# Kernel tuning notes

Measured on AMD Instinct MI355X. Metric: run time of the kernel, lower is better.

Reference implementation:

```python
import jax, jax.numpy as jnp
import numpy as np

EMBED_DIM = 1024
NUM_HEADS = 16
HEAD_DIM = 64
B, S = 4, 2048


def setup_inputs() -> dict:
    key = jax.random.key(0)
    ks = jax.random.split(key, 5)
    std = 0.02
    x = jax.random.normal(ks[0], (B, S, EMBED_DIM), dtype=jnp.float32)
    Wq = std * jax.random.normal(ks[1], (NUM_HEADS, EMBED_DIM, HEAD_DIM), dtype=jnp.float32)
    Wk = std * jax.random.normal(ks[2], (NUM_HEADS, EMBED_DIM, HEAD_DIM), dtype=jnp.float32)
    Wv = std * jax.random.normal(ks[3], (NUM_HEADS, EMBED_DIM, HEAD_DIM), dtype=jnp.float32)
    Wo = std * jax.random.normal(ks[4], (NUM_HEADS, HEAD_DIM, EMBED_DIM), dtype=jnp.float32)
    bq = jnp.zeros((NUM_HEADS, HEAD_DIM), dtype=jnp.float32)
    bk = jnp.zeros((NUM_HEADS, HEAD_DIM), dtype=jnp.float32)
    bv = jnp.zeros((NUM_HEADS, HEAD_DIM), dtype=jnp.float32)
    bo = jnp.zeros((EMBED_DIM,), dtype=jnp.float32)
    return {"x": x, "Wq": Wq, "bq": bq, "Wk": Wk, "bk": bk,
            "Wv": Wv, "bv": bv, "Wo": Wo, "bo": bo}


def reference(x, Wq, bq, Wk, bk, Wv, bv, Wo, bo):
    # q,k,v: [b, s, n, h]
    q = jnp.einsum('bsd,ndh->bsnh', x, Wq) + bq
    k = jnp.einsum('bsd,ndh->bsnh', x, Wk) + bk
    v = jnp.einsum('bsd,ndh->bsnh', x, Wv) + bv
    scale = 1.0 / (HEAD_DIM ** 0.5)
    # non-causal full attention matrix [b, n, s, t]
    attn = jnp.einsum('bsnh,btnh->bnst', q, k) * scale
    attn = jax.nn.softmax(attn, axis=-1)
    after = jnp.einsum('bnst,btnh->bsnh', attn, v)
    out = jnp.einsum('bsnh,nhd->bsd', after, Wo) + bo
    return out
```

## Files before the change

### kernel.cpp

```cpp
#include <hip/hip_runtime.h>

typedef __bf16 bf16;
typedef bf16 bf16x8 __attribute__((ext_vector_type(8)));
typedef bf16 bf16x4 __attribute__((ext_vector_type(4)));
typedef bf16 bf16x2 __attribute__((ext_vector_type(2)));
typedef float f32x4 __attribute__((ext_vector_type(4)));
typedef float f32x16 __attribute__((ext_vector_type(16)));
typedef unsigned int u32;
typedef u32 u32x4 __attribute__((ext_vector_type(4)));
typedef int i32x2 __attribute__((ext_vector_type(2)));

constexpr int Bb = 4, Ss = 2048, Dd = 1024, NH = 16, HD = 64;
constexpr int BS = Bb * Ss;
constexpr float CSC = 0.18033688011112042f;

__device__ __forceinline__ int sw(int row, int col) {
  return (row << 6) + (col ^ ((row & 7) << 3));
}
__device__ __forceinline__ int sw128(int row, int col) {
  return (row << 7) + (col ^ ((row & 7) << 3));
}

__device__ __forceinline__ void g2l16(const bf16* g, bf16* l) {
  __builtin_amdgcn_global_load_lds(
      (const __attribute__((address_space(1))) void*)g,
      (__attribute__((address_space(3))) void*)l, 16, 0, 0);
}

__device__ __forceinline__ u32 pkbf(float a, float b) {
  bf16x2 v = {(bf16)a, (bf16)b};
  return __builtin_bit_cast(u32, v);
}

__global__ void prep(const float* __restrict__ x, bf16* __restrict__ xb,
                     const float* __restrict__ Wq, const float* __restrict__ Wk,
                     const float* __restrict__ Wv, const float* __restrict__ Wo,
                     const float* __restrict__ bq, const float* __restrict__ bk,
                     const float* __restrict__ bv,
                     bf16* __restrict__ WT_all, bf16* __restrict__ WoT,
                     float* __restrict__ bias_all) {
  __shared__ bf16 Ts[64 * 72];
  const int t = threadIdx.x;
  if (blockIdx.y == 0) {
    int o = (blockIdx.x * 256 + t) * 4;
    f32x4 v = *(const f32x4*)&x[o];
    bf16x4 r = {(bf16)v[0], (bf16)v[1], (bf16)v[2], (bf16)v[3]};
    *(bf16x4*)&xb[o] = r;
    return;
  }
  if (blockIdx.x > 1024) return;
  if (blockIdx.x == 1024) {
    for (int j = t; j < 3072; j += 256) {
      int s2 = j >> 10;
      const float* bb = (s2 == 0) ? bq : (s2 == 1) ? bk : bv;
      bias_all[j] = bb[j & 1023] * (s2 == 0 ? CSC : 1.0f);
    }
    return;
  }
  const int sel = blockIdx.x >> 8, bx = blockIdx.x & 255;
  if (sel < 3) {
    const float* W = (sel == 0) ? Wq : (sel == 1) ? Wk : Wv;
    float scale = (sel == 0) ? CSC : 1.0f;
    int head = bx >> 4, dt = bx & 15;
    const float* src = W + head * 65536 + dt * 64 * 64;
#pragma unroll
    for (int i = 0; i < 4; ++i) {
      int idx = i * 256 + t;
      int dr = idx >> 4, hc = (idx & 15) * 4;
      f32x4 v = *(const f32x4*)&src[dr * 64 + hc];
#pragma unroll
      for (int k = 0; k < 4; ++k) Ts[(hc + k) * 72 + dr] = (bf16)(v[k] * scale);
    }
    __syncthreads();
    bf16* dst = WT_all + (size_t)sel * 1048576 + (size_t)(head * 64) * 1024 + dt * 64;
#pragma unroll
    for (int i = 0; i < 2; ++i) {
      int idx = i * 256 + t;
      int hr = idx >> 3, ch = (idx & 7) * 8;
      *(bf16x8*)&dst[(size_t)hr * 1024 + ch] = *(const bf16x8*)&Ts[hr * 72 + ch];
    }
  } else {
    int ct = bx >> 4, dt = bx & 15;
    const float* src = Wo + (size_t)(ct * 64) * 1024 + dt * 64;
#pragma unroll
    for (int i = 0; i < 4; ++i) {
      int idx = i * 256 + t;
      int cr = idx >> 4, dc = (idx & 15) * 4;
      f32x4 v = *(const f32x4*)&src[(size_t)cr * 1024 + dc];
#pragma unroll
      for (int k = 0; k < 4; ++k) Ts[(dc + k) * 72 + cr] = (bf16)v[k];
    }
    __syncthreads();
    bf16* dst = WoT + (size_t)(dt * 64) * 1024 + ct * 64;
#pragma unroll
    for (int i = 0; i < 2; ++i) {
      int idx = i * 256 + t;
      int dr = idx >> 3, ch = (idx & 7) * 8;
      *(bf16x8*)&dst[(size_t)dr * 1024 + ch] = *(const bf16x8*)&Ts[dr * 72 + ch];
    }
  }
}

__device__ __forceinline__ void gemm_core(const bf16* __restrict__ A,
                                          const bf16* __restrict__ BT,
                                          int m0, int n0, bf16* As, bf16* Bs,
                                          f32x4 (&acc)[4][4]) {
  const int t = threadIdx.x;
  const int l = t & 63, q = l >> 4, lm = l & 15;
  const int w = t >> 6, wm = w & 1, wn = w >> 1;
  int ro[4], co[4];
#pragma unroll
  for (int i = 0; i < 4; ++i) {
    int o = i * 256 + t;
    ro[i] = o >> 3;
    co[i] = ((o & 7) ^ ((o >> 3) & 7)) << 3;
  }
  const int lbase = (t & 192) * 8;
  for (int k0 = 0; k0 < 1024; k0 += 64) {
    __syncthreads();
#pragma unroll
    for (int i = 0; i < 4; ++i)
      g2l16(&A[(size_t)(m0 + ro[i]) * 1024 + k0 + co[i]], &As[i * 2048 + lbase]);
#pragma unroll
    for (int i = 0; i < 4; ++i)
      g2l16(&BT[(size_t)(n0 + ro[i]) * 1024 + k0 + co[i]], &Bs[i * 2048 + lbase]);
    __syncthreads();
#pragma unroll
    for (int kh = 0; kh < 2; ++kh) {
      bf16x8 a[4], b[4];
#pragma unroll
      for (int i = 0; i < 4; ++i)
        a[i] = *(const bf16x8*)&As[sw(wm * 64 + i * 16 + lm, kh * 32 + q * 8)];
#pragma unroll
      for (int i = 0; i < 4; ++i)
        b[i] = *(const bf16x8*)&Bs[sw(wn * 64 + i * 16 + lm, kh * 32 + q * 8)];
#pragma unroll
      for (int mt = 0; mt < 4; ++mt)
#pragma unroll
        for (int nt = 0; nt < 4; ++nt)
          acc[mt][nt] = __builtin_amdgcn_mfma_f32_16x16x32_bf16(a[mt], b[nt], acc[mt][nt], 0, 0, 0);
    }
  }
}

__global__ __launch_bounds__(256) void gemm_qkv(const bf16* __restrict__ xb,
                                                const bf16* __restrict__ WT,
                                                const float* __restrict__ bias_all,
                                                bf16* __restrict__ QKb,
                                                bf16* __restrict__ VTb) {
  __shared__ __align__(16) bf16 SMEM[2 * 128 * 64];
  bf16* As = SMEM;
  bf16* Bs = SMEM + 128 * 64;
  const int bid = blockIdx.x;
  const int t = threadIdx.x;
  const int l = t & 63, q = l >> 4, lm = l & 15;
  const int w = t >> 6, wm = w & 1, wn = w >> 1;
  const bool vmode = bid >= 1024;
  int m0, n0;
  const bf16 *A, *BT;
  if (!vmode) {
    int xcd = bid & 7, idx = bid >> 3;
    m0 = (idx >> 1) * 128;
    n0 = (xcd * 2 + (idx & 1)) * 128;
    A = xb; BT = WT;
  } else {
    int b2 = bid - 1024;
    int xcd = b2 & 7, idx = b2 >> 3;
    m0 = (idx >> 3) * 128;
    n0 = (xcd * 8 + (idx & 7)) * 128;
    A = WT + (size_t)2048 * 1024; BT = xb;
  }
  f32x4 acc[4][4] = {};
  gemm_core(A, BT, m0, n0, As, Bs, acc);
  if (vmode) {
    __syncthreads();
#pragma unroll
    for (int nt = 0; nt < 4; ++nt) {
      int sl = wn * 64 + nt * 16 + lm;
#pragma unroll
      for (int mt = 0; mt < 4; ++mt) {
        int ml = wm * 64 + mt * 16 + q * 4;
#pragma unroll
        for (int r = 0; r < 4; ++r)
          SMEM[sw128(ml + r, sl)] = (bf16)(acc[mt][nt][r] + bias_all[2048 + m0 + ml + r]);
      }
    }
    __syncthreads();
    int hh = t >> 1, half = (t & 1) * 64;
    int m = m0 + hh;
    size_t gb = (size_t)((n0 >> 11) * 16 + (m >> 6)) * 131072 +
                (size_t)(m & 63) * 2048 + (n0 & 2047) + half;
#pragma unroll
    for (int k = 0; k < 8; ++k)
      *(bf16x8*)&VTb[gb + k * 8] = *(const bf16x8*)&SMEM[sw128(hh, half + k * 8)];
  } else {
#pragma unroll
    for (int nt = 0; nt < 4; ++nt) {
      int col = n0 + wn * 64 + nt * 16 + lm;
      float bb = bias_all[col];
#pragma unroll
      for (int mt = 0; mt < 4; ++mt) {
        int row = m0 + wm * 64 + mt * 16 + q * 4;
#pragma unroll
        for (int r = 0; r < 4; ++r)
          QKb[(size_t)(row + r) * 2048 + col] = (bf16)(acc[mt][nt][r] + bb);
      }
    }
  }
}

__global__ __launch_bounds__(256) void gemm_out(const bf16* __restrict__ after,
                                                const bf16* __restrict__ WoT,
                                                const float* __restrict__ bo,
                                                float* __restrict__ out) {
  __shared__ __align__(16) bf16 SMEM[2 * 128 * 64];
  const int bid = blockIdx.x;
  const int t = threadIdx.x;
  const int l = t & 63, q = l >> 4, lm = l & 15;
  const int w = t >> 6, wm = w & 1, wn = w >> 1;
  const int xcd = bid & 7, idx = bid >> 3;
  const int n0 = xcd * 128, m0 = idx * 128;
  f32x4 acc[4][4] = {};
  gemm_core(after, WoT, m0, n0, SMEM, SMEM + 128 * 64, acc);
#pragma unroll
  for (int nt = 0; nt < 4; ++nt) {
    int col = n0 + wn * 64 + nt * 16 + lm;
    float bb = bo[col];
#pragma unroll
    for (int mt = 0; mt < 4; ++mt) {
      int row = m0 + wm * 64 + mt * 16 + q * 4;
#pragma unroll
      for (int r = 0; r < 4; ++r)
        out[(size_t)(row + r) * 1024 + col] = acc[mt][nt][r] + bb;
    }
  }
}

__global__ __launch_bounds__(256, 2) void attn(const bf16* __restrict__ QK,
                                               const bf16* __restrict__ VT,
                                               bf16* __restrict__ after) {
  __shared__ __align__(16) bf16 SMEM[32768];
  const int t = threadIdx.x;
  const int l = t & 63, w = t >> 6;
  const int lh = l & 31, H = l >> 5;
  const int f = blockIdx.x;
  const int bn = (f & 7) | ((f >> 6) << 3);
  const int s0 = ((f >> 3) & 7) * 256;
  const int b = bn >> 4, n = bn & 15;
  const bf16* Qb = QK + (size_t)(b * 2048) * 2048 + n * 64;
  const bf16* Kb = Qb + 1024;
  const bf16* Vtb = VT + (size_t)bn * 131072;
  const int rr = t >> 3;
  const int co0 = ((t & 7) ^ (rr & 7)) << 3;
  const int lbase = (t & 192) * 8;
#pragma unroll
  for (int i = 0; i < 8; ++i)
    g2l16(&Qb[(size_t)(s0 + i * 32 + rr) * 2048 + co0], &SMEM[i * 2048 + lbase]);
  __syncthreads();
  bf16x8 qb[2][4];
#pragma unroll
  for (int qt = 0; qt < 2; ++qt)
#pragma unroll
    for (int ks = 0; ks < 4; ++ks)
      qb[qt][ks] = *(const bf16x8*)&SMEM[sw(w * 64 + qt * 32 + lh, ks * 16 + H * 8)];
  __syncthreads();
#pragma unroll
  for (int s = 0; s < 3; ++s)
#pragma unroll
    for (int i = 0; i < 2; ++i) {
      g2l16(&Kb[(size_t)(s * 64 + i * 32 + rr) * 2048 + co0],
            &SMEM[s * 4096 + i * 2048 + lbase]);
      g2l16(&Vtb[(size_t)(i * 32 + rr) * 2048 + s * 64 + co0],
            &SMEM[16384 + s * 4096 + i * 2048 + lbase]);
    }
  f32x16 o_acc[2][2] = {};
  float rsA[2] = {0.f, 0.f}, rsB[2] = {0.f, 0.f};
  for (int rd = 0; rd < 32; ++rd) {
    const int cur = rd & 3;
    const bf16* Ks = &SMEM[cur * 4096];
    const bf16* Vs = &SMEM[16384 + cur * 4096];
    if (rd < 30)       asm volatile("s_waitcnt vmcnt(8)" ::: "memory");
    else if (rd == 30) asm volatile("s_waitcnt vmcnt(4)" ::: "memory");
    else               asm volatile("s_waitcnt vmcnt(0)" ::: "memory");
    __builtin_amdgcn_s_barrier();
    __builtin_amdgcn_sched_barrier(0);
    if (rd <= 28) {
      int st = rd + 3, nb = st & 3, t0n = st * 64;
#pragma unroll
      for (int i = 0; i < 2; ++i) {
        g2l16(&Kb[(size_t)(t0n + i * 32 + rr) * 2048 + co0],
              &SMEM[nb * 4096 + i * 2048 + lbase]);
        g2l16(&Vtb[(size_t)(i * 32 + rr) * 2048 + t0n + co0],
              &SMEM[16384 + nb * 4096 + i * 2048 + lbase]);
      }
    }
#pragma unroll
    for (int tt = 0; tt < 2; ++tt) {
      bf16x8 kb[4];
#pragma unroll
      for (int ks = 0; ks < 4; ++ks)
        kb[ks] = *(const bf16x8*)&Ks[sw(tt * 32 + lh, ks * 16 + H * 8)];
      f32x16 sc[2] = {};
      __builtin_amdgcn_s_setprio(1);
#pragma unroll
      for (int ks = 0; ks < 4; ++ks)
#pragma unroll
        for (int qt = 0; qt < 2; ++qt)
          sc[qt] = __builtin_amdgcn_mfma_f32_32x32x16_bf16(kb[ks], qb[qt][ks], sc[qt], 0, 0, 0);
      __builtin_amdgcn_s_setprio(0);
      u32 pk[2][8];
#pragma unroll
      for (int qt = 0; qt < 2; ++qt)
#pragma unroll
        for (int i = 0; i < 8; ++i) {
          float p0 = __builtin_amdgcn_exp2f(sc[qt][2 * i]);
          float p1 = __builtin_amdgcn_exp2f(sc[qt][2 * i + 1]);
          rsA[qt] += p0;
          rsB[qt] += p1;
          pk[qt][i] = pkbf(p0, p1);
        }
#pragma unroll
      for (int ks2 = 0; ks2 < 2; ++ks2) {
        bf16x8 pa[2];
#pragma unroll
        for (int qt = 0; qt < 2; ++qt) {
          u32x4 av;
#if __has_builtin(__builtin_amdgcn_permlane32_swap)
          i32x2 sA = __builtin_amdgcn_permlane32_swap(
              (int)pk[qt][ks2 * 4 + 0], (int)pk[qt][ks2 * 4 + 2], false, false);
          i32x2 sB = __builtin_amdgcn_permlane32_swap(
              (int)pk[qt][ks2 * 4 + 1], (int)pk[qt][ks2 * 4 + 3], false, false);
          av[0] = (u32)sA[0]; av[1] = (u32)sB[0]; av[2] = (u32)sA[1]; av[3] = (u32)sB[1];
#else
          u32 xx[4];
          xx[0] = __shfl_xor((int)pk[qt][ks2 * 4 + 0], 32);
          xx[1] = __shfl_xor((int)pk[qt][ks2 * 4 + 1], 32);
          xx[2] = __shfl_xor((int)pk[qt][ks2 * 4 + 2], 32);
          xx[3] = __shfl_xor((int)pk[qt][ks2 * 4 + 3], 32);
          av[0] = H ? xx[2] : pk[qt][ks2 * 4 + 0];
          av[1] = H ? xx[3] : pk[qt][ks2 * 4 + 1];
          av[2] = H ? pk[qt][ks2 * 4 + 2] : xx[0];
          av[3] = H ? pk[qt][ks2 * 4 + 3] : xx[1];
#endif
          pa[qt] = __builtin_bit_cast(bf16x8, av);
        }
        __builtin_amdgcn_s_setprio(1);
#pragma unroll
        for (int ht = 0; ht < 2; ++ht) {
          bf16x8 vb = *(const bf16x8*)&Vs[sw(ht * 32 + lh, tt * 32 + ks2 * 16 + H * 8)];
#pragma unroll
          for (int qt = 0; qt < 2; ++qt)
            o_acc[qt][ht] = __builtin_amdgcn_mfma_f32_32x32x16_bf16(pa[qt], vb, o_acc[qt][ht], 0, 0, 0);
        }
        __builtin_amdgcn_s_setprio(0);
      }
    }
  }
#pragma unroll
  for (int qt = 0; qt < 2; ++qt) {
    float rs = rsA[qt] + rsB[qt];
    rs += __shfl_xor(rs, 32);
    float inv = 1.f / rs;
#pragma unroll
    for (int r = 0; r < 16; ++r) {
      int sl = (r & 3) + 8 * (r >> 2) + 4 * H;
      float invr = __shfl(inv, sl);
      size_t base = (size_t)(b * 2048 + s0 + w * 64 + qt * 32 + sl) * 1024 + n * 64;
#pragma unroll
      for (int ht = 0; ht < 2; ++ht)
        after[base + ht * 32 + lh] = (bf16)(o_acc[qt][ht][r] * invr);
    }
  }
}

extern "C" void kernel_launch(void* const* d_in, const int* in_sizes, int n_in,
                              void* d_out, int out_size, void* d_ws, size_t ws_size,
                              hipStream_t stream) {
  const float* x  = (const float*)d_in[0];
  const float* Wq = (const float*)d_in[1];
  const float* bq = (const float*)d_in[2];
  const float* Wk = (const float*)d_in[3];
  const float* bk = (const float*)d_in[4];
  const float* Wv = (const float*)d_in[5];
  const float* bv = (const float*)d_in[6];
  const float* Wo = (const float*)d_in[7];
  const float* bo = (const float*)d_in[8];
  float* out = (float*)d_out;

  bf16* WT_all    = (bf16*)d_ws;
  bf16* WoT       = WT_all + (size_t)3072 * 1024;
  float* bias_all = (float*)(WoT + (size_t)1024 * 1024);
  bf16* xb        = (bf16*)(bias_all + 4096);
  bf16* QKb       = xb + (size_t)BS * Dd;
  bf16* VTb       = QKb + (size_t)BS * 2048;
  bf16* after     = VTb + (size_t)Bb * NH * HD * Ss;

  prep<<<dim3(8192, 2), dim3(256), 0, stream>>>(x, xb, Wq, Wk, Wv, Wo, bq, bk, bv,
                                                WT_all, WoT, bias_all);
  gemm_qkv<<<dim3(1536), dim3(256), 0, stream>>>(xb, WT_all, bias_all, QKb, VTb);
  attn<<<dim3(512), dim3(256), 0, stream>>>(QKb, VTb, after);
  gemm_out<<<dim3(512), dim3(256), 0, stream>>>(after, WoT, bo, out);
}
```

Baseline: 278.5 us.

## Split QKV GEMM into 256x256-tile Q/K kernel with 8-wave pipelined schedule

Moves the Q/K projection into a new kernel that uses 256x256 output tiles, 512 threads, a 128KB double-buffered LDS layout, and staged loads interleaved with MFMA phases plus setprio hints. The V projection is split into its own launch. The larger tiles raise data reuse per loaded byte and the interleaved schedule is meant to hide global-load latency. The cost is an extra kernel launch, only 256 blocks for the Q/K grid, and heavy LDS use that limits occupancy.

New measurement: 264.9 us. 4.9% less time.

```diff
diff --git a/kernel.cpp b/kernel.cpp
--- a/kernel.cpp
+++ b/kernel.cpp
@@ -143,11 +143,161 @@
   }
 }
 
-__global__ __launch_bounds__(256) void gemm_qkv(const bf16* __restrict__ xb,
-                                                const bf16* __restrict__ WT,
-                                                const float* __restrict__ bias_all,
-                                                bf16* __restrict__ QKb,
-                                                bf16* __restrict__ VTb) {
+__global__ __launch_bounds__(512, 2) void gemm_qk8(const bf16* __restrict__ A,
+                                                   const bf16* __restrict__ BT,
+                                                   const float* __restrict__ bias_all,
+                                                   bf16* __restrict__ C) {
+  __shared__ __align__(16) bf16 SMEM[65536];
+  const int t = threadIdx.x;
+  const int l = t & 63, q = l >> 4, lm = l & 15;
+  const int w = t >> 6, wm = w & 1, wn = w >> 1;
+  const int bid = blockIdx.x;
+  const int xcd = bid & 7, cc = bid >> 3;
+  const int mt = xcd * 4 + (cc >> 3), nt = cc & 7;
+  const int m0 = mt * 256, n0 = nt * 256;
+  const bf16* Ag = A + (size_t)m0 * 1024;
+  const bf16* Bg = BT + (size_t)n0 * 1024;
+  const int sR = t >> 3;
+  const int sC = t & 7;
+  const int dstb = (t & 448) * 8;
+
+  auto stA = [&](int bufb, int h, int kt) {
+#pragma unroll
+    for (int i = 0; i < 2; ++i) {
+      int Lh = i * 64 + sR;
+      int gr = ((Lh >> 6) << 7) + h * 64 + (Lh & 63);
+      g2l16(&Ag[(size_t)gr * 1024 + kt * 64 + ((sC ^ (Lh & 7)) << 3)],
+            &SMEM[bufb * 32768 + h * 8192 + i * 4096 + dstb]);
+    }
+  };
+  auto stB = [&](int bufb, int h, int kt) {
+#pragma unroll
+    for (int i = 0; i < 2; ++i) {
+      int Lh = i * 64 + sR;
+      int gr = ((Lh >> 5) << 6) + h * 32 + (Lh & 31);
+      g2l16(&Bg[(size_t)gr * 1024 + kt * 64 + ((sC ^ (Lh & 7)) << 3)],
+            &SMEM[bufb * 32768 + 16384 + h * 8192 + i * 4096 + dstb]);
+    }
+  };
+  auto rdA = [&](int base, int mt16, int ks) {
+    int L = ((mt16 >> 2) << 7) + wm * 64 + ((mt16 & 3) << 4) + lm;
+    return *(const bf16x8*)&SMEM[base + sw(L, ks * 32 + q * 8)];
+  };
+  auto rdB = [&](int base, int nt16, int ks) {
+    int L = ((nt16 >> 1) << 7) + wn * 32 + ((nt16 & 1) << 4) + lm;
+    return *(const bf16x8*)&SMEM[base + 16384 + sw(L, ks * 32 + q * 8)];
+  };
+
+  stA(0, 0, 0); stA(0, 1, 0); stB(0, 0, 0); stB(0, 1, 0);
+  stA(1, 0, 1); stB(1, 0, 1);
+  asm volatile("s_waitcnt vmcnt(4)" ::: "memory");
+  __builtin_amdgcn_s_barrier();
+  __builtin_amdgcn_sched_barrier(0);
+
+  f32x4 acc[8][4] = {};
+  int cur = 0;
+  for (int kt = 0; kt < 16; ++kt, cur ^= 1) {
+    const int base = cur * 32768;
+    bf16x8 af[4][2], b0[2][2], b1[2][2];
+#pragma unroll
+    for (int mi = 0; mi < 4; ++mi)
+#pragma unroll
+      for (int ks = 0; ks < 2; ++ks) af[mi][ks] = rdA(base, mi, ks);
+#pragma unroll
+    for (int ni = 0; ni < 2; ++ni)
+#pragma unroll
+      for (int ks = 0; ks < 2; ++ks) b0[ni][ks] = rdB(base, ni, ks);
+    if (kt + 1 < 16) { stA(cur ^ 1, 1, kt + 1); stB(cur ^ 1, 1, kt + 1); }
+    __builtin_amdgcn_s_barrier();
+    __builtin_amdgcn_s_setprio(1);
+#pragma unroll
+    for (int mi = 0; mi < 4; ++mi)
+#pragma unroll
+      for (int ni = 0; ni < 2; ++ni)
+#pragma unroll
+        for (int ks = 0; ks < 2; ++ks)
+          acc[mi][ni] = __builtin_amdgcn_mfma_f32_16x16x32_bf16(af[mi][ks], b0[ni][ks], acc[mi][ni], 0, 0, 0);
+    __builtin_amdgcn_s_setprio(0);
+    __builtin_amdgcn_sched_barrier(0);
+    __builtin_amdgcn_s_barrier();
+    __builtin_amdgcn_sched_barrier(0);
+#pragma unroll
+    for (int ni = 0; ni < 2; ++ni)
+#pragma unroll
+      for (int ks = 0; ks < 2; ++ks) b1[ni][ks] = rdB(base, 2 + ni, ks);
+    __builtin_amdgcn_s_barrier();
+    __builtin_amdgcn_s_setprio(1);
+#pragma unroll
+    for (int mi = 0; mi < 4; ++mi)
+#pragma unroll
+      for (int ni = 0; ni < 2; ++ni)
+#pragma unroll
+        for (int ks = 0; ks < 2; ++ks)
+          acc[mi][2 + ni] = __builtin_amdgcn_mfma_f32_16x16x32_bf16(af[mi][ks], b1[ni][ks], acc[mi][2 + ni], 0, 0, 0);
+    __builtin_amdgcn_s_setprio(0);
+    __builtin_amdgcn_sched_barrier(0);
+    __builtin_amdgcn_s_barrier();
+    __builtin_amdgcn_sched_barrier(0);
+#pragma unroll
+    for (int mi = 0; mi < 4; ++mi)
+#pragma unroll
+      for (int ks = 0; ks < 2; ++ks) af[mi][ks] = rdA(base, 4 + mi, ks);
+#pragma unroll
+    for (int ni = 0; ni < 2; ++ni)
+#pragma unroll
+      for (int ks = 0; ks < 2; ++ks) b0[ni][ks] = rdB(base, ni, ks);
+    if (kt + 2 < 16) stA(cur, 0, kt + 2);
+    __builtin_amdgcn_s_barrier();
+    __builtin_amdgcn_s_setprio(1);
+#pragma unroll
+    for (int mi = 0; mi < 4; ++mi)
+#pragma unroll
+      for (int ni = 0; ni < 2; ++ni)
+#pragma unroll
+        for (int ks = 0; ks < 2; ++ks)
+          acc[4 + mi][ni] = __builtin_amdgcn_mfma_f32_16x16x32_bf16(af[mi][ks], b0[ni][ks], acc[4 + mi][ni], 0, 0, 0);
+    __builtin_amdgcn_s_setprio(0);
+    __builtin_amdgcn_sched_barrier(0);
+    __builtin_amdgcn_s_barrier();
+    __builtin_amdgcn_sched_barrier(0);
+#pragma unroll
+    for (int ni = 0; ni < 2; ++ni)
+#pragma unroll
+      for (int ks = 0; ks < 2; ++ks) b1[ni][ks] = rdB(base, 2 + ni, ks);
+    if (kt + 2 < 16) stB(cur, 0, kt + 2);
+    __builtin_amdgcn_s_barrier();
+    __builtin_amdgcn_s_setprio(1);
+#pragma unroll
+    for (int mi = 0; mi < 4; ++mi)
+#pragma unroll
+      for (int ni = 0; ni < 2; ++ni)
+#pragma unroll
+        for (int ks = 0; ks < 2; ++ks)
+          acc[4 + mi][2 + ni] = __builtin_amdgcn_mfma_f32_16x16x32_bf16(af[mi][ks], b1[ni][ks], acc[4 + mi][2 + ni], 0, 0, 0);
+    __builtin_amdgcn_s_setprio(0);
+    asm volatile("s_waitcnt vmcnt(4)" ::: "memory");
+    __builtin_amdgcn_sched_barrier(0);
+    __builtin_amdgcn_s_barrier();
+    __builtin_amdgcn_sched_barrier(0);
+  }
+#pragma unroll
+  for (int mi = 0; mi < 8; ++mi) {
+    int row = m0 + wm * 128 + mi * 16 + q * 4;
+#pragma unroll
+    for (int ni = 0; ni < 4; ++ni) {
+      int col = n0 + wn * 64 + ni * 16 + lm;
+      float bb = bias_all[col];
+#pragma unroll
+      for (int r = 0; r < 4; ++r)
+        C[(size_t)(row + r) * 2048 + col] = (bf16)(acc[mi][ni][r] + bb);
+    }
+  }
+}
+
+__global__ __launch_bounds__(256) void gemm_v(const bf16* __restrict__ xb,
+                                              const bf16* __restrict__ WT,
+                                              const float* __restrict__ bias_all,
+                                              bf16* __restrict__ VTb) {
   __shared__ __align__(16) bf16 SMEM[2 * 128 * 64];
   bf16* As = SMEM;
   bf16* Bs = SMEM + 128 * 64;
@@ -155,58 +305,33 @@
   const int t = threadIdx.x;
   const int l = t & 63, q = l >> 4, lm = l & 15;
   const int w = t >> 6, wm = w & 1, wn = w >> 1;
-  const bool vmode = bid >= 1024;
-  int m0, n0;
-  const bf16 *A, *BT;
-  if (!vmode) {
-    int xcd = bid & 7, idx = bid >> 3;
-    m0 = (idx >> 1) * 128;
-    n0 = (xcd * 2 + (idx & 1)) * 128;
-    A = xb; BT = WT;
-  } else {
-    int b2 = bid - 1024;
-    int xcd = b2 & 7, idx = b2 >> 3;
-    m0 = (idx >> 3) * 128;
-    n0 = (xcd * 8 + (idx & 7)) * 128;
-    A = WT + (size_t)2048 * 1024; BT = xb;
-  }
+  const int xcd = bid & 7, idx = bid >> 3;
+  const int m0 = (idx >> 3) * 128;
+  const int n0 = (xcd * 8 + (idx & 7)) * 128;
+  const bf16* A = WT + (size_t)2048 * 1024;
+  const bf16* BT = xb;
   f32x4 acc[4][4] = {};
   gemm_core(A, BT, m0, n0, As, Bs, acc);
-  if (vmode) {
-    __syncthreads();
-#pragma unroll
-    for (int nt = 0; nt < 4; ++nt) {
-      int sl = wn * 64 + nt * 16 + lm;
-#pragma unroll
-      for (int mt = 0; mt < 4; ++mt) {
-        int ml = wm * 64 + mt * 16 + q * 4;
-#pragma unroll
-        for (int r = 0; r < 4; ++r)
-          SMEM[sw128(ml + r, sl)] = (bf16)(acc[mt][nt][r] + bias_all[2048 + m0 + ml + r]);
-      }
-    }
-    __syncthreads();
-    int hh = t >> 1, half = (t & 1) * 64;
-    int m = m0 + hh;
-    size_t gb = (size_t)((n0 >> 11) * 16 + (m >> 6)) * 131072 +
-                (size_t)(m & 63) * 2048 + (n0 & 2047) + half;
-#pragma unroll
-    for (int k = 0; k < 8; ++k)
-      *(bf16x8*)&VTb[gb + k * 8] = *(const bf16x8*)&SMEM[sw128(hh, half + k * 8)];
-  } else {
-#pragma unroll
-    for (int nt = 0; nt < 4; ++nt) {
-      int col = n0 + wn * 64 + nt * 16 + lm;
-      float bb = bias_all[col];
-#pragma unroll
-      for (int mt = 0; mt < 4; ++mt) {
-        int row = m0 + wm * 64 + mt * 16 + q * 4;
-#pragma unroll
-        for (int r = 0; r < 4; ++r)
-          QKb[(size_t)(row + r) * 2048 + col] = (bf16)(acc[mt][nt][r] + bb);
-      }
-    }
-  }
+  __syncthreads();
+#pragma unroll
+  for (int nt = 0; nt < 4; ++nt) {
+    int sl = wn * 64 + nt * 16 + lm;
+#pragma unroll
+    for (int mt = 0; mt < 4; ++mt) {
+      int ml = wm * 64 + mt * 16 + q * 4;
+#pragma unroll
+      for (int r = 0; r < 4; ++r)
+        SMEM[sw128(ml + r, sl)] = (bf16)(acc[mt][nt][r] + bias_all[2048 + m0 + ml + r]);
+    }
+  }
+  __syncthreads();
+  int hh = t >> 1, half = (t & 1) * 64;
+  int m = m0 + hh;
+  size_t gb = (size_t)((n0 >> 11) * 16 + (m >> 6)) * 131072 +
+              (size_t)(m & 63) * 2048 + (n0 & 2047) + half;
+#pragma unroll
+  for (int k = 0; k < 8; ++k)
+    *(bf16x8*)&VTb[gb + k * 8] = *(const bf16x8*)&SMEM[sw128(hh, half + k * 8)];
 }
 
 __global__ __launch_bounds__(256) void gemm_out(const bf16* __restrict__ after,
@@ -397,7 +522,8 @@
 
   prep<<<dim3(8192, 2), dim3(256), 0, stream>>>(x, xb, Wq, Wk, Wv, Wo, bq, bk, bv,
                                                 WT_all, WoT, bias_all);
-  gemm_qkv<<<dim3(1536), dim3(256), 0, stream>>>(xb, WT_all, bias_all, QKb, VTb);
+  gemm_qk8<<<dim3(256), dim3(512), 0, stream>>>(xb, WT_all, bias_all, QKb);
+  gemm_v<<<dim3(512), dim3(256), 0, stream>>>(xb, WT_all, bias_all, VTb);
   attn<<<dim3(512), dim3(256), 0, stream>>>(QKb, VTb, after);
   gemm_out<<<dim3(512), dim3(256), 0, stream>>>(after, WoT, bo, out);
 }
```
